# Kernel tuning notes

Measured on AMD Instinct MI355X. Metric: run time of the kernel, lower is better.

Reference implementation:

```python
import jax, jax.numpy as jnp
import numpy as np


def setup_inputs() -> dict:
    key = jax.random.key(0)
    k1, k2, k3, k4 = jax.random.split(key, 4)
    H, D, Dh, NH = 4096, 1024, 256, 4  # height, weight1, INNER_FEATURE_A, heads
    x = jax.random.normal(k1, (H, D), dtype=jnp.float32)
    Wq = jax.random.normal(k2, (NH, D, Dh), dtype=jnp.float32)
    lin_w = jax.random.normal(k3, (D, NH * Dh), dtype=jnp.float32)  # torch Linear weight [out, in]
    lin_b = jax.random.normal(k4, (D,), dtype=jnp.float32)
    return {"x": x, "Wq": Wq, "lin_w": lin_w, "lin_b": lin_b}


def reference(x, Wq, lin_w, lin_b):
    # Faithful to source: Q = K = V = x @ Wq1 (original uses Wq1 for all three).
    # mask_flag=False -> multiplicative all-ones mask (identity, elided).
    # qkv: [heads, H, Dh]
    qkv = jnp.einsum('hd,ndk->nhk', x, Wq)
    # scores: [heads, H, H]; softmax over dim=1 of the 2D matrix = last axis here
    scores = jnp.einsum('nqk,npk->nqp', qkv, qkv)
    attn = jax.nn.softmax(scores, axis=-1)
    z = jnp.einsum('nqp,npk->nqk', attn, qkv)  # [heads, H, Dh]
    # concat heads along feature dim -> [H, heads*Dh]
    zc = jnp.transpose(z, (1, 0, 2)).reshape(x.shape[0], -1)
    return zc @ lin_w.T + lin_b
```

## Files before the change

kernel.cpp:

```cpp
#include <hip/hip_runtime.h>
#include <math.h>

#define SEQ 4096
#define DIM 1024
#define DHEAD 256
#define NHEADS 4

typedef __attribute__((ext_vector_type(8))) short bf16x8;
typedef __attribute__((ext_vector_type(4))) float f32x4;
typedef __attribute__((ext_vector_type(4))) short short4v;
typedef __attribute__((ext_vector_type(8))) short short8v;

__device__ __forceinline__ unsigned short f2b(float f) {
    union { float f; unsigned u; } v; v.f = f;
    unsigned r = v.u + 0x7FFFu + ((v.u >> 16) & 1u);
    return (unsigned short)(r >> 16);
}
__device__ __forceinline__ float b2f(unsigned short u) {
    union { unsigned u; float f; } v; v.u = ((unsigned)u) << 16;
    return v.f;
}

__device__ __forceinline__ void gll16(const void* g, void* lds) {
    __builtin_amdgcn_global_load_lds(
        (const __attribute__((address_space(1))) unsigned*)g,
        (__attribute__((address_space(3))) unsigned*)lds, 16, 0, 0);
}

__device__ __forceinline__ f32x4 mfma16(bf16x8 a, bf16x8 b, f32x4 c) {
    return __builtin_amdgcn_mfma_f32_16x16x32_bf16(a, b, c, 0, 0, 0);
}

__global__ __launch_bounds__(256)
void conv_kernel(const float* __restrict__ in, unsigned short* __restrict__ out, int n4) {
    int i = blockIdx.x * 256 + threadIdx.x;
    if (i >= n4) return;
    float4 v = ((const float4*)in)[i];
    short4v o;
    o[0] = (short)f2b(v.x); o[1] = (short)f2b(v.y);
    o[2] = (short)f2b(v.z); o[3] = (short)f2b(v.w);
    *(short4v*)(out + (size_t)i * 4) = o;
}

__global__ __launch_bounds__(256)
void wqt_kernel(const float* __restrict__ Wq, unsigned short* __restrict__ WqT) {
    __shared__ unsigned short T[64][72];
    const int tid = threadIdx.x;
    const int h = blockIdx.z;
    const int d0 = blockIdx.x * 64, c0 = blockIdx.y * 64;
#pragma unroll
    for (int it = 0; it < 4; ++it) {
        int f = tid + 256 * it;
        int row = f >> 4, cg = f & 15;
        float4 v = *(const float4*)&Wq[((size_t)(h * DIM + d0 + row)) * DHEAD + c0 + cg * 4];
        T[row][cg * 4 + 0] = f2b(v.x); T[row][cg * 4 + 1] = f2b(v.y);
        T[row][cg * 4 + 2] = f2b(v.z); T[row][cg * 4 + 3] = f2b(v.w);
    }
    __syncthreads();
#pragma unroll
    for (int it = 0; it < 2; ++it) {
        int f = tid + 256 * it;
        int cl = f >> 3, dg = f & 7;
        short8v o;
#pragma unroll
        for (int e = 0; e < 8; ++e) o[e] = (short)T[dg * 8 + e][cl];
        *(short8v*)&WqT[((size_t)(h * DHEAD + c0 + cl)) * DIM + d0 + dg * 8] = o;
    }
}

__global__ __launch_bounds__(256)
void qkvt_kernel(const unsigned short* __restrict__ qkv, unsigned short* __restrict__ qkvT) {
    __shared__ unsigned short T[64][72];
    const int tid = threadIdx.x;
    const int h = blockIdx.z;
    const int r0 = blockIdx.x * 64, c0 = blockIdx.y * 64;
#pragma unroll
    for (int it = 0; it < 2; ++it) {
        int f = tid + 256 * it;
        int row = f >> 3, cg = f & 7;
        short8v v = *(const short8v*)&qkv[((size_t)h * SEQ + r0 + row) * DHEAD + c0 + cg * 8];
#pragma unroll
        for (int e = 0; e < 8; ++e) T[row][cg * 8 + e] = (unsigned short)v[e];
    }
    __syncthreads();
#pragma unroll
    for (int it = 0; it < 2; ++it) {
        int f = tid + 256 * it;
        int cl = f >> 3, rg = f & 7;
        short8v o;
#pragma unroll
        for (int e = 0; e < 8; ++e) o[e] = (short)T[rg * 8 + e][cl];
        *(short8v*)&qkvT[((size_t)h * DHEAD + c0 + cl) * SEQ + r0 + rg * 8] = o;
    }
}

__global__ __launch_bounds__(256)
void qkv_gemm_kernel(const unsigned short* __restrict__ A,
                     const unsigned short* __restrict__ B,
                     unsigned short* __restrict__ qkv) {
    __shared__ unsigned short As[128 * 64];
    __shared__ unsigned short Bs[128 * 64];
    const int tid = threadIdx.x, w = tid >> 6, l = tid & 63;
    const int g = l >> 4, r16 = l & 15;
    const int m0 = blockIdx.x * 128, n0 = blockIdx.y * 128;
    const int wm = (w >> 1) * 64, wn = (w & 1) * 64;

    f32x4 acc[4][4];
#pragma unroll
    for (int mr = 0; mr < 4; ++mr)
#pragma unroll
        for (int nr = 0; nr < 4; ++nr) acc[mr][nr] = (f32x4){0.f, 0.f, 0.f, 0.f};

    for (int kb = 0; kb < DIM; kb += 64) {
        __syncthreads();
#pragma unroll
        for (int cc = 0; cc < 4; ++cc) {
            int row = w * 32 + cc * 8 + (l >> 3);
            int c = (l & 7) ^ (row & 7);
            gll16(&A[(size_t)(m0 + row) * DIM + kb + c * 8], &As[(size_t)(w * 32 + cc * 8) * 64]);
            gll16(&B[(size_t)(n0 + row) * DIM + kb + c * 8], &Bs[(size_t)(w * 32 + cc * 8) * 64]);
        }
        __syncthreads();
#pragma unroll
        for (int s = 0; s < 2; ++s) {
            bf16x8 af[4], bf[4];
#pragma unroll
            for (int mr = 0; mr < 4; ++mr) {
                int row = wm + mr * 16 + r16;
                int st = (s * 4 + g) ^ (row & 7);
                af[mr] = *(const bf16x8*)&As[row * 64 + st * 8];
            }
#pragma unroll
            for (int nr = 0; nr < 4; ++nr) {
                int row = wn + nr * 16 + r16;
                int st = (s * 4 + g) ^ (row & 7);
                bf[nr] = *(const bf16x8*)&Bs[row * 64 + st * 8];
            }
#pragma unroll
            for (int mr = 0; mr < 4; ++mr)
#pragma unroll
                for (int nr = 0; nr < 4; ++nr)
                    acc[mr][nr] = mfma16(af[mr], bf[nr], acc[mr][nr]);
        }
    }
#pragma unroll
    for (int mr = 0; mr < 4; ++mr)
#pragma unroll
        for (int nr = 0; nr < 4; ++nr) {
            int n = n0 + wn + nr * 16 + r16;
            int h = n >> 8, c = n & 255;
#pragma unroll
            for (int r = 0; r < 4; ++r) {
                int m = m0 + wm + mr * 16 + g * 4 + r;
                qkv[((size_t)h * SEQ + m) * DHEAD + c] = f2b(acc[mr][nr][r]);
            }
        }
}

__global__ __launch_bounds__(256, 2)
void attn_kernel(const unsigned short* __restrict__ qkv,
                 const unsigned short* __restrict__ qkvT,
                 unsigned short* __restrict__ p0,
                 unsigned short* __restrict__ p1,
                 float* __restrict__ ml) {
    __shared__ unsigned short Ks[64 * 256];
    __shared__ unsigned short Vt[256 * 64];
    __shared__ unsigned short Ps[64 * 64];
    __shared__ float alphaS[64];
    __shared__ float mS[64], lS[64];

    const int tid = threadIdx.x, w = tid >> 6, l = tid & 63;
    const int g = l >> 4, r16 = l & 15;
    const int bid = blockIdx.x;
    const int h = (bid & 7) >> 1, hf = bid & 1;
    const int qb = bid >> 3;
    const unsigned short* __restrict__ qh = qkv + (size_t)h * SEQ * DHEAD;
    const unsigned short* __restrict__ qth = qkvT + (size_t)h * DHEAD * SEQ;
    const int jb0 = hf * (SEQ / 2);
    const int NT = (SEQ / 2) / 64;

    bf16x8 qf[8];
    {
        const unsigned short* qrow = qh + (size_t)(qb * 64 + w * 16 + r16) * DHEAD + g * 8;
#pragma unroll
        for (int s = 0; s < 8; ++s) qf[s] = *(const bf16x8*)(qrow + s * 32);
    }

    f32x4 Oacc[16];
#pragma unroll
    for (int i = 0; i < 16; ++i) Oacc[i] = (f32x4){0.f, 0.f, 0.f, 0.f};
    float mrow = -INFINITY, lrow = 0.f;

    for (int t = 0; t < NT; ++t) {
        const int jb = jb0 + t * 64;
        __syncthreads();
#pragma unroll
        for (int cc = 0; cc < 8; ++cc) {
            int ch = w * 8 + cc;
            int j = ch * 2 + (l >> 5);
            int cp = l & 31;
            int c = (cp & 24) | ((cp & 7) ^ (j & 7));
            gll16(&qh[(size_t)(jb + j) * DHEAD + c * 8], &Ks[(size_t)ch * 512]);
        }
#pragma unroll
        for (int cc = 0; cc < 8; ++cc) {
            int ch = w * 8 + cc;
            int d = ch * 8 + (l >> 3);
            int c = (l & 7) ^ (d & 7);
            gll16(&qth[(size_t)d * SEQ + jb + c * 8], &Vt[(size_t)ch * 512]);
        }
        __syncthreads();

        f32x4 sacc[4];
#pragma unroll
        for (int jt = 0; jt < 4; ++jt) sacc[jt] = (f32x4){0.f, 0.f, 0.f, 0.f};
        __builtin_amdgcn_s_setprio(1);
#pragma unroll
        for (int s = 0; s < 8; ++s)
#pragma unroll
            for (int jt = 0; jt < 4; ++jt) {
                int j = jt * 16 + r16;
                int c = s * 4 + g;
                int st = (c & 24) | ((c & 7) ^ (j & 7));
                bf16x8 af = *(const bf16x8*)&Ks[j * 256 + st * 8];
                sacc[jt] = mfma16(af, qf[s], sacc[jt]);
            }
        __builtin_amdgcn_s_setprio(0);

        float mx = sacc[0][0];
#pragma unroll
        for (int jt = 0; jt < 4; ++jt)
#pragma unroll
            for (int r = 0; r < 4; ++r) mx = fmaxf(mx, sacc[jt][r]);
        mx = fmaxf(mx, __shfl_xor(mx, 16, 64));
        mx = fmaxf(mx, __shfl_xor(mx, 32, 64));

        float mn = fmaxf(mrow, mx);
        float alpha = __expf(mrow - mn);
        mrow = mn;

        float rsum = 0.f;
        short4v pf[4];
#pragma unroll
        for (int jt = 0; jt < 4; ++jt)
#pragma unroll
            for (int r = 0; r < 4; ++r) {
                float p = __expf(sacc[jt][r] - mrow);
                rsum += p;
                pf[jt][r] = (short)f2b(p);
            }
        rsum += __shfl_xor(rsum, 16, 64);
        rsum += __shfl_xor(rsum, 32, 64);
        lrow = lrow * alpha + rsum;

#pragma unroll
        for (int jt = 0; jt < 4; ++jt) {
            int st = (jt * 2 + (g >> 1)) ^ (r16 & 7);
            *(short4v*)&Ps[(w * 16 + r16) * 64 + st * 8 + (g & 1) * 4] = pf[jt];
        }
        if (g == 0) alphaS[w * 16 + r16] = alpha;
        __syncthreads();

        bf16x8 pa[8];
#pragma unroll
        for (int qs = 0; qs < 4; ++qs) {
            f32x4 av = *(const f32x4*)&alphaS[qs * 16 + g * 4];
#pragma unroll
            for (int dt = 0; dt < 4; ++dt)
#pragma unroll
                for (int r = 0; r < 4; ++r) Oacc[qs * 4 + dt][r] *= av[r];
#pragma unroll
            for (int s2 = 0; s2 < 2; ++s2) {
                int qrow = qs * 16 + r16;
                int st = (s2 * 4 + g) ^ (qrow & 7);
                pa[qs * 2 + s2] = *(const bf16x8*)&Ps[qrow * 64 + st * 8];
            }
        }
        __builtin_amdgcn_s_setprio(1);
#pragma unroll
        for (int dt = 0; dt < 4; ++dt) {
            int d = w * 64 + dt * 16 + r16;
#pragma unroll
            for (int s2 = 0; s2 < 2; ++s2) {
                int st = (s2 * 4 + g) ^ (d & 7);
                bf16x8 bv = *(const bf16x8*)&Vt[d * 64 + st * 8];
#pragma unroll
                for (int qs = 0; qs < 4; ++qs)
                    Oacc[qs * 4 + dt] = mfma16(pa[qs * 2 + s2], bv, Oacc[qs * 4 + dt]);
            }
        }
        __builtin_amdgcn_s_setprio(0);
    }

    if (g == 0) { mS[w * 16 + r16] = mrow; lS[w * 16 + r16] = lrow; }
    __syncthreads();
    unsigned short* po = hf ? p1 : p0;
#pragma unroll
    for (int qs = 0; qs < 4; ++qs)
#pragma unroll
        for (int dt = 0; dt < 4; ++dt) {
            int d = w * 64 + dt * 16 + r16;
#pragma unroll
            for (int r = 0; r < 4; ++r) {
                int q = qb * 64 + qs * 16 + g * 4 + r;
                po[(size_t)q * (NHEADS * DHEAD) + h * DHEAD + d] = f2b(Oacc[qs * 4 + dt][r]);
            }
        }
    if (tid < 64) {
        int q = qb * 64 + tid;
        float* mlq = ml + ((size_t)(hf * NHEADS + h) * SEQ + q) * 2;
        mlq[0] = mS[tid]; mlq[1] = lS[tid];
    }
}

__global__ __launch_bounds__(256)
void combine_kernel(const unsigned short* __restrict__ pa,
                    const unsigned short* __restrict__ pb,
                    const float* __restrict__ ml,
                    unsigned short* __restrict__ zc) {
    size_t t = (size_t)blockIdx.x * 256 + threadIdx.x;
    size_t f = t * 8;
    int q = (int)(f >> 10);
    int h = (int)((f >> 8) & 3);
    const float* ml0 = ml + ((size_t)h * SEQ + q) * 2;
    const float* ml1 = ml + ((size_t)(NHEADS + h) * SEQ + q) * 2;
    float m0 = ml0[0], l0 = ml0[1], m1 = ml1[0], l1 = ml1[1];
    float M = fmaxf(m0, m1);
    float e0 = __expf(m0 - M), e1 = __expf(m1 - M);
    float inv = 1.f / (e0 * l0 + e1 * l1);
    e0 *= inv; e1 *= inv;
    short8v a = *(const short8v*)(pa + f);
    short8v b = *(const short8v*)(pb + f);
    short8v o;
#pragma unroll
    for (int e = 0; e < 8; ++e)
        o[e] = (short)f2b(e0 * b2f((unsigned short)a[e]) + e1 * b2f((unsigned short)b[e]));
    *(short8v*)(zc + f) = o;
}

__global__ __launch_bounds__(256)
void out_gemm_kernel(const unsigned short* __restrict__ A,
                     const unsigned short* __restrict__ B,
                     const float* __restrict__ lb, float* __restrict__ out) {
    __shared__ unsigned short As[128 * 64];
    __shared__ unsigned short Bs[128 * 64];
    const int tid = threadIdx.x, w = tid >> 6, l = tid & 63;
    const int g = l >> 4, r16 = l & 15;
    const int m0 = blockIdx.x * 128, n0 = blockIdx.y * 128;
    const int wm = (w >> 1) * 64, wn = (w & 1) * 64;

    f32x4 acc[4][4];
#pragma unroll
    for (int mr = 0; mr < 4; ++mr)
#pragma unroll
        for (int nr = 0; nr < 4; ++nr) acc[mr][nr] = (f32x4){0.f, 0.f, 0.f, 0.f};

    for (int kb = 0; kb < DIM; kb += 64) {
        __syncthreads();
#pragma unroll
        for (int cc = 0; cc < 4; ++cc) {
            int row = w * 32 + cc * 8 + (l >> 3);
            int c = (l & 7) ^ (row & 7);
            gll16(&A[(size_t)(m0 + row) * DIM + kb + c * 8], &As[(size_t)(w * 32 + cc * 8) * 64]);
            gll16(&B[(size_t)(n0 + row) * DIM + kb + c * 8], &Bs[(size_t)(w * 32 + cc * 8) * 64]);
        }
        __syncthreads();
#pragma unroll
        for (int s = 0; s < 2; ++s) {
            bf16x8 af[4], bf[4];
#pragma unroll
            for (int mr = 0; mr < 4; ++mr) {
                int row = wm + mr * 16 + r16;
                int st = (s * 4 + g) ^ (row & 7);
                af[mr] = *(const bf16x8*)&As[row * 64 + st * 8];
            }
#pragma unroll
            for (int nr = 0; nr < 4; ++nr) {
                int row = wn + nr * 16 + r16;
                int st = (s * 4 + g) ^ (row & 7);
                bf[nr] = *(const bf16x8*)&Bs[row * 64 + st * 8];
            }
#pragma unroll
            for (int mr = 0; mr < 4; ++mr)
#pragma unroll
                for (int nr = 0; nr < 4; ++nr)
                    acc[mr][nr] = mfma16(af[mr], bf[nr], acc[mr][nr]);
        }
    }
#pragma unroll
    for (int mr = 0; mr < 4; ++mr)
#pragma unroll
        for (int nr = 0; nr < 4; ++nr) {
            int n = n0 + wn + nr * 16 + r16;
            float bv = lb[n];
#pragma unroll
            for (int r = 0; r < 4; ++r) {
                int m = m0 + wm + mr * 16 + g * 4 + r;
                out[(size_t)m * DIM + n] = acc[mr][nr][r] + bv;
            }
        }
}

extern "C" void kernel_launch(void* const* d_in, const int* in_sizes, int n_in,
                              void* d_out, int out_size, void* d_ws, size_t ws_size,
                              hipStream_t stream) {
    const float* x  = (const float*)d_in[0];
    const float* Wq = (const float*)d_in[1];
    const float* lw = (const float*)d_in[2];
    const float* lb = (const float*)d_in[3];
    float* out = (float*)d_out;

    char* wsb = (char*)d_ws;
    unsigned short* qkvb = (unsigned short*)(wsb);
    unsigned short* qkvT = (unsigned short*)(wsb + ((size_t)8 << 20));
    unsigned short* xb   = (unsigned short*)(wsb + ((size_t)16 << 20));
    unsigned short* p0   = xb;
    unsigned short* WqT  = (unsigned short*)(wsb + ((size_t)24 << 20));
    float*          ml   = (float*)(wsb + ((size_t)24 << 20));
    unsigned short* lwb  = (unsigned short*)(wsb + ((size_t)26 << 20));
    unsigned short* p1   = (unsigned short*)d_out;

    conv_kernel<<<4096, 256, 0, stream>>>(x, xb, (SEQ * DIM) / 4);
    conv_kernel<<<1024, 256, 0, stream>>>(lw, lwb, (DIM * DIM) / 4);
    wqt_kernel<<<dim3(16, 4, 4), 256, 0, stream>>>(Wq, WqT);
    qkv_gemm_kernel<<<dim3(SEQ / 128, DIM / 128), 256, 0, stream>>>(xb, WqT, qkvb);
    qkvt_kernel<<<dim3(64, 4, 4), 256, 0, stream>>>(qkvb, qkvT);
    attn_kernel<<<512, 256, 0, stream>>>(qkvb, qkvT, p0, p1, ml);
    combine_kernel<<<(SEQ * DIM / 8) / 256, 256, 0, stream>>>(p0, p1, ml, p0);
    out_gemm_kernel<<<dim3(SEQ / 128, DIM / 128), 256, 0, stream>>>(p0, lwb, lb, out);
}
```

Before: 165.4 us.

## Double-buffer K/V tiles, enlarge query tile per block, skip lazy rescale

Result: slower. 207.4 us (+25.4%).

```diff
diff --git a/kernel.cpp b/kernel.cpp
--- a/kernel.cpp
+++ b/kernel.cpp
@@ -157,17 +157,15 @@
         }
 }
 
-__global__ __launch_bounds__(256, 2)
+__global__ __launch_bounds__(256, 1)
 void attn_kernel(const unsigned short* __restrict__ qkv,
                  const unsigned short* __restrict__ qkvT,
                  unsigned short* __restrict__ p0,
                  unsigned short* __restrict__ p1,
                  float* __restrict__ ml) {
-    __shared__ unsigned short Ks[64 * 256];
-    __shared__ unsigned short Vt[256 * 64];
-    __shared__ unsigned short Ps[64 * 64];
-    __shared__ float alphaS[64];
-    __shared__ float mS[64], lS[64];
+    __shared__ unsigned short Ks[2][64 * 256];
+    __shared__ unsigned short Vt[2][256 * 64];
+    __shared__ unsigned short Ps[4][32 * 64];
 
     const int tid = threadIdx.x, w = tid >> 6, l = tid & 63;
     const int g = l >> 4, r16 = l & 15;
@@ -179,41 +177,54 @@
     const int jb0 = hf * (SEQ / 2);
     const int NT = (SEQ / 2) / 64;
 
-    bf16x8 qf[8];
-    {
-        const unsigned short* qrow = qh + (size_t)(qb * 64 + w * 16 + r16) * DHEAD + g * 8;
-#pragma unroll
-        for (int s = 0; s < 8; ++s) qf[s] = *(const bf16x8*)(qrow + s * 32);
-    }
-
-    f32x4 Oacc[16];
-#pragma unroll
-    for (int i = 0; i < 16; ++i) Oacc[i] = (f32x4){0.f, 0.f, 0.f, 0.f};
-    float mrow = -INFINITY, lrow = 0.f;
+    bf16x8 qf[2][8];
+#pragma unroll
+    for (int qs = 0; qs < 2; ++qs) {
+        const unsigned short* qrow =
+            qh + (size_t)(qb * 128 + w * 32 + qs * 16 + r16) * DHEAD + g * 8;
+#pragma unroll
+        for (int s = 0; s < 8; ++s) qf[qs][s] = *(const bf16x8*)(qrow + s * 32);
+    }
+
+#define STAGEKV(buf, jb)                                                            \
+    {                                                                               \
+        _Pragma("unroll")                                                           \
+        for (int cc = 0; cc < 8; ++cc) {                                            \
+            int ch = w * 8 + cc;                                                    \
+            int j = ch * 2 + (l >> 5);                                              \
+            int cp = l & 31;                                                        \
+            int c = (cp & 24) | ((cp & 7) ^ (j & 7));                               \
+            gll16(&qh[(size_t)((jb) + j) * DHEAD + c * 8], &Ks[buf][(size_t)ch * 512]); \
+        }                                                                           \
+        _Pragma("unroll")                                                           \
+        for (int cc = 0; cc < 8; ++cc) {                                            \
+            int ch = w * 8 + cc;                                                    \
+            int d = ch * 8 + (l >> 3);                                              \
+            int c = (l & 7) ^ (d & 7);                                              \
+            gll16(&qth[(size_t)d * SEQ + (jb) + c * 8], &Vt[buf][(size_t)ch * 512]); \
+        }                                                                           \
+    }
+
+    STAGEKV(0, jb0);
+
+    f32x4 Oacc[2][16];
+#pragma unroll
+    for (int qs = 0; qs < 2; ++qs)
+#pragma unroll
+        for (int dt = 0; dt < 16; ++dt) Oacc[qs][dt] = (f32x4){0.f, 0.f, 0.f, 0.f};
+    float mrow[2] = {-INFINITY, -INFINITY}, lrow[2] = {0.f, 0.f};
 
     for (int t = 0; t < NT; ++t) {
-        const int jb = jb0 + t * 64;
+        const int cur = t & 1;
         __syncthreads();
-#pragma unroll
-        for (int cc = 0; cc < 8; ++cc) {
-            int ch = w * 8 + cc;
-            int j = ch * 2 + (l >> 5);
-            int cp = l & 31;
-            int c = (cp & 24) | ((cp & 7) ^ (j & 7));
-            gll16(&qh[(size_t)(jb + j) * DHEAD + c * 8], &Ks[(size_t)ch * 512]);
-        }
-#pragma unroll
-        for (int cc = 0; cc < 8; ++cc) {
-            int ch = w * 8 + cc;
-            int d = ch * 8 + (l >> 3);
-            int c = (l & 7) ^ (d & 7);
-            gll16(&qth[(size_t)d * SEQ + jb + c * 8], &Vt[(size_t)ch * 512]);
-        }
-        __syncthreads();
-
-        f32x4 sacc[4];
-#pragma unroll
-        for (int jt = 0; jt < 4; ++jt) sacc[jt] = (f32x4){0.f, 0.f, 0.f, 0.f};
+        if (t + 1 < NT) STAGEKV(cur ^ 1, jb0 + (t + 1) * 64);
+
+        const unsigned short* Kb = &Ks[cur][0];
+        f32x4 sacc[2][4];
+#pragma unroll
+        for (int qs = 0; qs < 2; ++qs)
+#pragma unroll
+            for (int jt = 0; jt < 4; ++jt) sacc[qs][jt] = (f32x4){0.f, 0.f, 0.f, 0.f};
         __builtin_amdgcn_s_setprio(1);
 #pragma unroll
         for (int s = 0; s < 8; ++s)
@@ -222,94 +233,111 @@
                 int j = jt * 16 + r16;
                 int c = s * 4 + g;
                 int st = (c & 24) | ((c & 7) ^ (j & 7));
-                bf16x8 af = *(const bf16x8*)&Ks[j * 256 + st * 8];
-                sacc[jt] = mfma16(af, qf[s], sacc[jt]);
+                bf16x8 af = *(const bf16x8*)&Kb[j * 256 + st * 8];
+                sacc[0][jt] = mfma16(af, qf[0][s], sacc[0][jt]);
+                sacc[1][jt] = mfma16(af, qf[1][s], sacc[1][jt]);
             }
         __builtin_amdgcn_s_setprio(0);
 
-        float mx = sacc[0][0];
-#pragma unroll
-        for (int jt = 0; jt < 4; ++jt)
-#pragma unroll
-            for (int r = 0; r < 4; ++r) mx = fmaxf(mx, sacc[jt][r]);
-        mx = fmaxf(mx, __shfl_xor(mx, 16, 64));
-        mx = fmaxf(mx, __shfl_xor(mx, 32, 64));
-
-        float mn = fmaxf(mrow, mx);
-        float alpha = __expf(mrow - mn);
-        mrow = mn;
-
-        float rsum = 0.f;
-        short4v pf[4];
-#pragma unroll
-        for (int jt = 0; jt < 4; ++jt)
+#pragma unroll
+        for (int qs = 0; qs < 2; ++qs) {
+            float mx = sacc[qs][0][0];
+#pragma unroll
+            for (int jt = 0; jt < 4; ++jt)
+#pragma unroll
+                for (int r = 0; r < 4; ++r) mx = fmaxf(mx, sacc[qs][jt][r]);
+            mx = fmaxf(mx, __shfl_xor(mx, 16, 64));
+            mx = fmaxf(mx, __shfl_xor(mx, 32, 64));
+
+            bool needr = !__all(mx <= mrow[qs] + 8.f);
+            float alpha = 1.f;
+            if (needr) {
+                float mn = fmaxf(mrow[qs], mx);
+                alpha = __expf(mrow[qs] - mn);
+                mrow[qs] = mn;
+            }
+
+            float rsum = 0.f;
+            short4v pf[4];
+#pragma unroll
+            for (int jt = 0; jt < 4; ++jt)
+#pragma unroll
+                for (int r = 0; r < 4; ++r) {
+                    float p = __expf(sacc[qs][jt][r] - mrow[qs]);
+                    rsum += p;
+                    pf[jt][r] = (short)f2b(p);
+                }
+            rsum += __shfl_xor(rsum, 16, 64);
+            rsum += __shfl_xor(rsum, 32, 64);
+            lrow[qs] = lrow[qs] * alpha + rsum;
+
+#pragma unroll
+            for (int jt = 0; jt < 4; ++jt) {
+                int st = (2 * jt + (g >> 1)) ^ (r16 & 7);
+                *(short4v*)&Ps[w][(qs * 16 + r16) * 64 + st * 8 + (g & 1) * 4] = pf[jt];
+            }
+
+            if (needr) {
+                float av[4];
+#pragma unroll
+                for (int r = 0; r < 4; ++r) av[r] = __shfl(alpha, 4 * g + r, 64);
+#pragma unroll
+                for (int dt = 0; dt < 16; ++dt)
+#pragma unroll
+                    for (int r = 0; r < 4; ++r) Oacc[qs][dt][r] *= av[r];
+            }
+        }
+
+        asm volatile("s_waitcnt lgkmcnt(0)" ::: "memory");
+        __builtin_amdgcn_sched_barrier(0);
+
+        bf16x8 pa[2][2];
+#pragma unroll
+        for (int qs = 0; qs < 2; ++qs)
+#pragma unroll
+            for (int s2 = 0; s2 < 2; ++s2) {
+                int st = (4 * s2 + g) ^ (r16 & 7);
+                pa[qs][s2] = *(const bf16x8*)&Ps[w][(qs * 16 + r16) * 64 + st * 8];
+            }
+
+        const unsigned short* Vb = &Vt[cur][0];
+        __builtin_amdgcn_s_setprio(1);
+#pragma unroll
+        for (int dt = 0; dt < 16; ++dt) {
+            int d = dt * 16 + r16;
+#pragma unroll
+            for (int s2 = 0; s2 < 2; ++s2) {
+                int st = (4 * s2 + g) ^ (r16 & 7);
+                bf16x8 bv = *(const bf16x8*)&Vb[d * 64 + st * 8];
+                Oacc[0][dt] = mfma16(pa[0][s2], bv, Oacc[0][dt]);
+                Oacc[1][dt] = mfma16(pa[1][s2], bv, Oacc[1][dt]);
+            }
+        }
+        __builtin_amdgcn_s_setprio(0);
+    }
+#undef STAGEKV
+
+    asm volatile("s_waitcnt vmcnt(0)" ::: "memory");
+
+    unsigned short* po = hf ? p1 : p0;
+#pragma unroll
+    for (int qs = 0; qs < 2; ++qs)
+#pragma unroll
+        for (int dt = 0; dt < 16; ++dt) {
+            int d = dt * 16 + r16;
 #pragma unroll
             for (int r = 0; r < 4; ++r) {
-                float p = __expf(sacc[jt][r] - mrow);
-                rsum += p;
-                pf[jt][r] = (short)f2b(p);
-            }
-        rsum += __shfl_xor(rsum, 16, 64);
-        rsum += __shfl_xor(rsum, 32, 64);
-        lrow = lrow * alpha + rsum;
-
-#pragma unroll
-        for (int jt = 0; jt < 4; ++jt) {
-            int st = (jt * 2 + (g >> 1)) ^ (r16 & 7);
-            *(short4v*)&Ps[(w * 16 + r16) * 64 + st * 8 + (g & 1) * 4] = pf[jt];
-        }
-        if (g == 0) alphaS[w * 16 + r16] = alpha;
-        __syncthreads();
-
-        bf16x8 pa[8];
-#pragma unroll
-        for (int qs = 0; qs < 4; ++qs) {
-            f32x4 av = *(const f32x4*)&alphaS[qs * 16 + g * 4];
-#pragma unroll
-            for (int dt = 0; dt < 4; ++dt)
-#pragma unroll
-                for (int r = 0; r < 4; ++r) Oacc[qs * 4 + dt][r] *= av[r];
-#pragma unroll
-            for (int s2 = 0; s2 < 2; ++s2) {
-                int qrow = qs * 16 + r16;
-                int st = (s2 * 4 + g) ^ (qrow & 7);
-                pa[qs * 2 + s2] = *(const bf16x8*)&Ps[qrow * 64 + st * 8];
-            }
-        }
-        __builtin_amdgcn_s_setprio(1);
-#pragma unroll
-        for (int dt = 0; dt < 4; ++dt) {
-            int d = w * 64 + dt * 16 + r16;
-#pragma unroll
-            for (int s2 = 0; s2 < 2; ++s2) {
-                int st = (s2 * 4 + g) ^ (d & 7);
-                bf16x8 bv = *(const bf16x8*)&Vt[d * 64 + st * 8];
-#pragma unroll
-                for (int qs = 0; qs < 4; ++qs)
-                    Oacc[qs * 4 + dt] = mfma16(pa[qs * 2 + s2], bv, Oacc[qs * 4 + dt]);
-            }
-        }
-        __builtin_amdgcn_s_setprio(0);
-    }
-
-    if (g == 0) { mS[w * 16 + r16] = mrow; lS[w * 16 + r16] = lrow; }
-    __syncthreads();
-    unsigned short* po = hf ? p1 : p0;
-#pragma unroll
-    for (int qs = 0; qs < 4; ++qs)
-#pragma unroll
-        for (int dt = 0; dt < 4; ++dt) {
-            int d = w * 64 + dt * 16 + r16;
-#pragma unroll
-            for (int r = 0; r < 4; ++r) {
-                int q = qb * 64 + qs * 16 + g * 4 + r;
-                po[(size_t)q * (NHEADS * DHEAD) + h * DHEAD + d] = f2b(Oacc[qs * 4 + dt][r]);
-            }
-        }
-    if (tid < 64) {
-        int q = qb * 64 + tid;
-        float* mlq = ml + ((size_t)(hf * NHEADS + h) * SEQ + q) * 2;
-        mlq[0] = mS[tid]; mlq[1] = lS[tid];
+                int q = qb * 128 + w * 32 + qs * 16 + 4 * g + r;
+                po[(size_t)q * (NHEADS * DHEAD) + h * DHEAD + d] = f2b(Oacc[qs][dt][r]);
+            }
+        }
+    if (g == 0) {
+#pragma unroll
+        for (int qs = 0; qs < 2; ++qs) {
+            int q = qb * 128 + w * 32 + qs * 16 + r16;
+            float* mlq = ml + ((size_t)(hf * NHEADS + h) * SEQ + q) * 2;
+            mlq[0] = mrow[qs]; mlq[1] = lrow[qs];
+        }
     }
 }
 
@@ -425,7 +453,7 @@
     wqt_kernel<<<dim3(16, 4, 4), 256, 0, stream>>>(Wq, WqT);
     qkv_gemm_kernel<<<dim3(SEQ / 128, DIM / 128), 256, 0, stream>>>(xb, WqT, qkvb);
     qkvt_kernel<<<dim3(64, 4, 4), 256, 0, stream>>>(qkvb, qkvT);
-    attn_kernel<<<512, 256, 0, stream>>>(qkvb, qkvT, p0, p1, ml);
+    attn_kernel<<<256, 256, 0, stream>>>(qkvb, qkvT, p0, p1, ml);
     combine_kernel<<<(SEQ * DIM / 8) / 256, 256, 0, stream>>>(p0, p1, ml, p0);
     out_gemm_kernel<<<dim3(SEQ / 128, DIM / 128), 256, 0, stream>>>(p0, lwb, lb, out);
 }
```

## Prefetch next K/V tiles during compute and skip redundant softmax rescaling

Applied to the files above, without the earlier changes.

Result: slower. 172.7 us (+4.4%).

```diff
diff --git a/kernel.cpp b/kernel.cpp
--- a/kernel.cpp
+++ b/kernel.cpp
@@ -186,30 +186,43 @@
         for (int s = 0; s < 8; ++s) qf[s] = *(const bf16x8*)(qrow + s * 32);
     }
 
+#define STAGEK(jb)                                                                  \
+    {                                                                               \
+        _Pragma("unroll")                                                           \
+        for (int cc = 0; cc < 8; ++cc) {                                            \
+            int ch = w * 8 + cc;                          \
+            int j = ch * 2 + (l >> 5);                                              \
+            int cp = l & 31;                                                        \
+            int c = (cp & 24) | ((cp & 7) ^ (j & 7));                               \
+            gll16(&qh[(size_t)((jb) + j) * DHEAD + c * 8], &Ks[(size_t)ch * 512]);  \
+        }                                                                           \
+    }
+#define STAGEV(jb)                                                                  \
+    {                                                                               \
+        _Pragma("unroll")                                                           \
+        for (int cc = 0; cc < 8; ++cc) {                                            \
+            int ch = w * 8 + cc;                         \
+            int d = ch * 8 + (l >> 3);                                              \
+            int c = (l & 7) ^ (d & 7);                                              \
+            gll16(&qth[(size_t)d * SEQ + (jb) + c * 8], &Vt[(size_t)ch * 512]);     \
+        }                                                                           \
+    }
+
+    STAGEK(jb0);
+    STAGEV(jb0);
+
     f32x4 Oacc[16];
 #pragma unroll
     for (int i = 0; i < 16; ++i) Oacc[i] = (f32x4){0.f, 0.f, 0.f, 0.f};
     float mrow = -INFINITY, lrow = 0.f;
 
     for (int t = 0; t < NT; ++t) {
-        const int jb = jb0 + t * 64;
-        __syncthreads();
-#pragma unroll
-        for (int cc = 0; cc < 8; ++cc) {
-            int ch = w * 8 + cc;
-            int j = ch * 2 + (l >> 5);
-            int cp = l & 31;
-            int c = (cp & 24) | ((cp & 7) ^ (j & 7));
-            gll16(&qh[(size_t)(jb + j) * DHEAD + c * 8], &Ks[(size_t)ch * 512]);
-        }
-#pragma unroll
-        for (int cc = 0; cc < 8; ++cc) {
-            int ch = w * 8 + cc;
-            int d = ch * 8 + (l >> 3);
-            int c = (l & 7) ^ (d & 7);
-            gll16(&qth[(size_t)d * SEQ + jb + c * 8], &Vt[(size_t)ch * 512]);
-        }
-        __syncthreads();
+        const int jbn = jb0 + (t + 1) * 64;
+
+        __builtin_amdgcn_sched_barrier(0);
+        asm volatile("s_waitcnt vmcnt(8)" ::: "memory");
+        __builtin_amdgcn_s_barrier();
+        __builtin_amdgcn_sched_barrier(0);
 
         f32x4 sacc[4];
 #pragma unroll
@@ -227,6 +240,12 @@
             }
         __builtin_amdgcn_s_setprio(0);
 
+        __builtin_amdgcn_sched_barrier(0);
+        __builtin_amdgcn_s_barrier();
+        __builtin_amdgcn_sched_barrier(0);
+        if (t + 1 < NT) STAGEK(jbn);
+        __builtin_amdgcn_sched_barrier(0);
+
         float mx = sacc[0][0];
 #pragma unroll
         for (int jt = 0; jt < 4; ++jt)
@@ -235,9 +254,12 @@
         mx = fmaxf(mx, __shfl_xor(mx, 16, 64));
         mx = fmaxf(mx, __shfl_xor(mx, 32, 64));
 
-        float mn = fmaxf(mrow, mx);
-        float alpha = __expf(mrow - mn);
-        mrow = mn;
+        float alpha = 1.f;
+        if (!__all(mx <= mrow + 8.f)) {
+            float mn = fmaxf(mrow, mx);
+            alpha = __expf(mrow - mn);
+            mrow = mn;
+        }
 
         float rsum = 0.f;
         short4v pf[4];
@@ -255,20 +277,27 @@
 
 #pragma unroll
         for (int jt = 0; jt < 4; ++jt) {
-            int st = (jt * 2 + (g >> 1)) ^ (r16 & 7);
+            int st = (2 * jt + (g >> 1)) ^ (r16 & 7);
             *(short4v*)&Ps[(w * 16 + r16) * 64 + st * 8 + (g & 1) * 4] = pf[jt];
         }
         if (g == 0) alphaS[w * 16 + r16] = alpha;
-        __syncthreads();
+
+        __builtin_amdgcn_sched_barrier(0);
+        if (t + 1 < NT) { asm volatile("s_waitcnt vmcnt(8) lgkmcnt(0)" ::: "memory"); }
+        else            { asm volatile("s_waitcnt vmcnt(0) lgkmcnt(0)" ::: "memory"); }
+        __builtin_amdgcn_s_barrier();
+        __builtin_amdgcn_sched_barrier(0);
 
         bf16x8 pa[8];
 #pragma unroll
         for (int qs = 0; qs < 4; ++qs) {
             f32x4 av = *(const f32x4*)&alphaS[qs * 16 + g * 4];
-#pragma unroll
-            for (int dt = 0; dt < 4; ++dt)
-#pragma unroll
-                for (int r = 0; r < 4; ++r) Oacc[qs * 4 + dt][r] *= av[r];
+            if (!__all((av[0] == 1.f) & (av[1] == 1.f) & (av[2] == 1.f) & (av[3] == 1.f))) {
+#pragma unroll
+                for (int dt = 0; dt < 4; ++dt)
+#pragma unroll
+                    for (int r = 0; r < 4; ++r) Oacc[qs * 4 + dt][r] *= av[r];
+            }
 #pragma unroll
             for (int s2 = 0; s2 < 2; ++s2) {
                 int qrow = qs * 16 + r16;
@@ -290,7 +319,17 @@
             }
         }
         __builtin_amdgcn_s_setprio(0);
-    }
+
+        __builtin_amdgcn_sched_barrier(0);
+        __builtin_amdgcn_s_barrier();
+        __builtin_amdgcn_sched_barrier(0);
+        if (t + 1 < NT) STAGEV(jbn);
+        __builtin_amdgcn_sched_barrier(0);
+    }
+#undef STAGEK
+#undef STAGEV
+
+    asm volatile("s_waitcnt vmcnt(0)" ::: "memory");
 
     if (g == 0) { mS[w * 16 + r16] = mrow; lS[w * 16 + r16] = lrow; }
     __syncthreads();
```
